# Kernel optimization log

Measured on AMD Instinct MI355X. Metric: run time of the kernel, lower is better.

Reference implementation:

```python
import jax, jax.numpy as jnp
import numpy as np

B, C, H, W = 8, 64, 64, 64
R = 4
INTER = C // R   # 16
QK = C // 8      # 8
OUT = 64
EPS = 1e-5

def _bn(h, s, b, m, v):
    # inference-mode BatchNorm2d over channel dim of NCHW
    inv = s / jnp.sqrt(v + EPS)
    return h * inv[None, :, None, None] + (b - m * inv)[None, :, None, None]

def _conv1x1(h, w, b):
    # 1x1 conv == per-pixel matmul over channels
    return jnp.einsum('oc,bchw->bohw', w, h) + b[None, :, None, None]

def setup_inputs() -> dict:
    key = jax.random.key(0)
    ks = jax.random.split(key, 16)
    def wgt(k, shape):
        return jax.random.normal(k, shape, jnp.float32) * 0.05
    ones = lambda n: jnp.ones((n,), jnp.float32)
    zeros = lambda n: jnp.zeros((n,), jnp.float32)
    return {
        'x': jax.random.normal(ks[0], (B, C, H, W), jnp.float32),
        'lw1': wgt(ks[1], (INTER, C)), 'lb1': zeros(INTER),
        'ls1': ones(INTER), 'lbb1': zeros(INTER), 'lm1': zeros(INTER), 'lv1': ones(INTER),
        'lw2': wgt(ks[2], (C, INTER)), 'lb2': zeros(C),
        'ls2': ones(C), 'lbb2': zeros(C), 'lm2': zeros(C), 'lv2': ones(C),
        'gw1': wgt(ks[3], (INTER, C)), 'gb1': zeros(INTER),
        'gs1': ones(INTER), 'gbb1': zeros(INTER), 'gm1': zeros(INTER), 'gv1': ones(INTER),
        'gw2': wgt(ks[4], (C, INTER)), 'gb2': zeros(C),
        'gs2': ones(C), 'gbb2': zeros(C), 'gm2': zeros(C), 'gv2': ones(C),
        'qw': wgt(ks[5], (QK, C)), 'qb': zeros(QK),
        'kw': wgt(ks[6], (QK, C)), 'kb': zeros(QK),
        'vw': wgt(ks[7], (C, C)), 'vb': zeros(C),
        'gamma': jnp.zeros((1,), jnp.float32),  # torch init: zeros
        'cw': wgt(ks[8], (OUT, C, 3, 3)), 'cb': zeros(OUT),
        'cs': ones(OUT), 'cbb': zeros(OUT), 'cm': zeros(OUT), 'cv': ones(OUT),
    }

def reference(x, lw1, lb1, ls1, lbb1, lm1, lv1, lw2, lb2, ls2, lbb2, lm2, lv2,
              gw1, gb1, gs1, gbb1, gm1, gv1, gw2, gb2, gs2, gbb2, gm2, gv2,
              qw, qb, kw, kb, vw, vb, gamma, cw, cb, cs, cbb, cm, cv):
    # --- SE-style channel gating: local branch (per-pixel) + global branch (GAP) ---
    xl = _bn(_conv1x1(jax.nn.relu(_bn(_conv1x1(x, lw1, lb1), ls1, lbb1, lm1, lv1)), lw2, lb2),
             ls2, lbb2, lm2, lv2)
    g = x.mean(axis=(2, 3), keepdims=True)  # AdaptiveAvgPool2d(1) -> [B,C,1,1]
    xg = _bn(_conv1x1(jax.nn.relu(_bn(_conv1x1(g, gw1, gb1), gs1, gbb1, gm1, gv1)), gw2, gb2),
             gs2, gbb2, gm2, gv2)
    xo = x * jax.nn.sigmoid(xl + xg)
    # --- full spatial self-attention (bmm -> softmax -> bmm, unscaled) ---
    # NOTE: the original forward computes this, forms gamma*out + xo, then
    # immediately overwrites `out` with conv(xo); we reproduce that faithfully.
    b_, c_, h_, w_ = x.shape
    n = h_ * w_
    q = _conv1x1(x, qw, qb).reshape(b_, QK, n)
    k = _conv1x1(x, kw, kb).reshape(b_, QK, n)
    att = jax.nn.softmax(jnp.einsum('bcn,bcm->bnm', q, k), axis=-1)  # [B,N,N]
    v = _conv1x1(x, vw, vb).reshape(b_, c_, n)
    attn_out = jnp.einsum('bcm,bnm->bcn', v, att).reshape(b_, c_, h_, w_)
    _dead = gamma[0] * attn_out + xo  # discarded by original module
    # --- final 3x3 conv + BN + ReLU applied to the gated features xo ---
    y = jax.lax.conv_general_dilated(xo, cw, (1, 1), 'SAME',
                                     dimension_numbers=('NCHW', 'OIHW', 'NCHW'))
    y = y + cb[None, :, None, None]
    return jax.nn.relu(_bn(y, cs, cbb, cm, cv))
```

## Files before the change

kernel.cpp:

```cpp
#include <hip/hip_runtime.h>
#include <hip/hip_bf16.h>

#define NPIX 4096
#define FEPS 1e-5f

typedef __hip_bfloat16 bf16;
typedef __attribute__((ext_vector_type(8))) short bf16x8;
typedef __attribute__((ext_vector_type(4))) float f32x4;

#define OFF_FOLD 64
#define OFF_G    512
#define OFF_LW1  1024
#define OFF_LW2  2048
#define OFF_GW1  3072
#define OFF_GW2  4096
#define WSWZ_BYTES_OFF 20480
#define XO_BYTES_OFF   94208

template<typename T> __device__ __forceinline__ float ldf(const T* p);
template<> __device__ __forceinline__ float ldf<bf16>(const bf16* p)  { return __bfloat162float(*p); }
template<> __device__ __forceinline__ float ldf<float>(const float* p){ return *p; }

template<typename T> __device__ __forceinline__ void stf(T* p, float v);
template<> __device__ __forceinline__ void stf<bf16>(bf16* p, float v)  { *p = __float2bfloat16(v); }
template<> __device__ __forceinline__ void stf<float>(float* p, float v){ *p = v; }

__device__ __forceinline__ unsigned short f2bu(float f) {
    union { bf16 h; unsigned short u; } c; c.h = __float2bfloat16(f); return c.u;
}
__device__ __forceinline__ float blo(unsigned u) {
    union { unsigned i; float f; } c; c.i = u << 16; return c.f;
}
__device__ __forceinline__ float bhi(unsigned u) {
    union { unsigned i; float f; } c; c.i = u & 0xffff0000u; return c.f;
}

__device__ __forceinline__ int probe_flag(const unsigned* __restrict__ x,
                                          int tid, int* sflag)
{
    if (tid < 64) {
        unsigned w = x[tid];
        unsigned h = w & 0xffffu;
        int e = (int)((h >> 7) & 0xff);
        int hit = (h == 0u || (e >= 96 && e <= 160)) ? 1 : 0;
        unsigned long long m = __ballot(hit);
        if (tid == 0) *sflag = (__popcll(m) >= 40) ? 1 : 2;
    }
    __syncthreads();
    return *sflag;
}

struct PrepArgs7 { const void* p[30]; };

template<typename T>
__device__ void prep_body(const PrepArgs7& a, float* __restrict__ ws,
                          unsigned short* __restrict__ wswz, int flag)
{
    const T* lw1  = (const T*)a.p[0];  const T* lb1  = (const T*)a.p[1];
    const T* ls1  = (const T*)a.p[2];  const T* lbb1 = (const T*)a.p[3];
    const T* lm1  = (const T*)a.p[4];  const T* lv1  = (const T*)a.p[5];
    const T* lw2  = (const T*)a.p[6];  const T* lb2  = (const T*)a.p[7];
    const T* ls2  = (const T*)a.p[8];  const T* lbb2 = (const T*)a.p[9];
    const T* lm2  = (const T*)a.p[10]; const T* lv2  = (const T*)a.p[11];
    const T* gw1  = (const T*)a.p[12]; const T* gb1  = (const T*)a.p[13];
    const T* gs1  = (const T*)a.p[14]; const T* gbb1 = (const T*)a.p[15];
    const T* gm1  = (const T*)a.p[16]; const T* gv1  = (const T*)a.p[17];
    const T* gw2  = (const T*)a.p[18]; const T* gb2  = (const T*)a.p[19];
    const T* gs2  = (const T*)a.p[20]; const T* gbb2 = (const T*)a.p[21];
    const T* gm2  = (const T*)a.p[22]; const T* gv2  = (const T*)a.p[23];
    const T* cw   = (const T*)a.p[24]; const T* cb   = (const T*)a.p[25];
    const T* cs   = (const T*)a.p[26]; const T* cbb  = (const T*)a.p[27];
    const T* cm   = (const T*)a.p[28]; const T* cv   = (const T*)a.p[29];

    int bx = blockIdx.x;
    int tid = threadIdx.x;
    if (bx < 16) {
        for (int e = tid; e < 2304; e += 256) {
            int E = bx * 2304 + e;
            int j = E & 7;
            int F = E >> 3;
            int l = F & 63;
            int g = (F >> 6) & 3;
            int ts = F >> 8;
            int s = ts & 1;
            int t = ts >> 1;
            int oc = g * 16 + (l & 15);
            int ic = s * 32 + (l >> 4) * 8 + j;
            wswz[E] = f2bu(ldf(cw + (oc * 64 + ic) * 9 + t));
        }
    } else if (bx == 16) {
        for (int e = tid; e < 4096; e += 256) {
            if (e < 1024)      ws[OFF_LW1 + e]        = ldf(lw1 + e);
            else if (e < 2048) ws[OFF_LW2 + e - 1024] = ldf(lw2 + e - 1024);
            else if (e < 3072) ws[OFF_GW1 + e - 2048] = ldf(gw1 + e - 2048);
            else               ws[OFF_GW2 + e - 3072] = ldf(gw2 + e - 3072);
        }
    } else {
        if (tid == 0) ((int*)ws)[0] = flag;
        if (tid < 16) {
            float inv = ldf(ls1 + tid) * rsqrtf(ldf(lv1 + tid) + FEPS);
            ws[OFF_FOLD + 0  + tid] = inv;
            ws[OFF_FOLD + 16 + tid] = ldf(lb1 + tid) * inv + ldf(lbb1 + tid) - ldf(lm1 + tid) * inv;
            float ginv = ldf(gs1 + tid) * rsqrtf(ldf(gv1 + tid) + FEPS);
            ws[OFF_FOLD + 160 + tid] = ginv;
            ws[OFF_FOLD + 176 + tid] = ldf(gb1 + tid) * ginv + ldf(gbb1 + tid) - ldf(gm1 + tid) * ginv;
        }
        if (tid < 64) {
            float inv2 = ldf(ls2 + tid) * rsqrtf(ldf(lv2 + tid) + FEPS);
            ws[OFF_FOLD + 32 + tid] = inv2;
            ws[OFF_FOLD + 96 + tid] = ldf(lb2 + tid) * inv2 + ldf(lbb2 + tid) - ldf(lm2 + tid) * inv2;
            float ginv2 = ldf(gs2 + tid) * rsqrtf(ldf(gv2 + tid) + FEPS);
            ws[OFF_FOLD + 192 + tid] = ginv2;
            ws[OFF_FOLD + 256 + tid] = ldf(gb2 + tid) * ginv2 + ldf(gbb2 + tid) - ldf(gm2 + tid) * ginv2;
            float cinv = ldf(cs + tid) * rsqrtf(ldf(cv + tid) + FEPS);
            ws[OFF_FOLD + 320 + tid] = cinv;
            ws[OFF_FOLD + 384 + tid] = ldf(cb + tid) * cinv + ldf(cbb + tid) - ldf(cm + tid) * cinv;
        }
    }
}

__global__ void r7_prep_means(PrepArgs7 a, const void* __restrict__ xv,
                              float* __restrict__ ws,
                              unsigned short* __restrict__ wswz)
{
    __shared__ int sflag;
    int t = threadIdx.x;
    int flag = probe_flag((const unsigned*)xv, t, &sflag);
    int bx = blockIdx.x;

    if (bx < 18) {
        if (flag == 1) prep_body<bf16>(a, ws, wswz, flag);
        else           prep_body<float>(a, ws, wswz, flag);
        return;
    }

    int bc = bx - 18;
    float s = 0.f;
    if (flag == 1) {
        const uint4* p = (const uint4*)((const bf16*)xv + (size_t)bc * NPIX);
#pragma unroll
        for (int i = 0; i < 2; ++i) {
            uint4 v = p[t * 2 + i];
            s += blo(v.x) + bhi(v.x) + blo(v.y) + bhi(v.y)
               + blo(v.z) + bhi(v.z) + blo(v.w) + bhi(v.w);
        }
    } else {
        const float4* p = (const float4*)((const float*)xv + (size_t)bc * NPIX);
#pragma unroll
        for (int i = 0; i < 4; ++i) {
            float4 v = p[t * 4 + i];
            s += v.x + v.y + v.z + v.w;
        }
    }
#pragma unroll
    for (int off = 32; off > 0; off >>= 1) s += __shfl_down(s, off, 64);
    __shared__ float red[4];
    if ((t & 63) == 0) red[t >> 6] = s;
    __syncthreads();
    if (t == 0)
        ws[OFF_G + bc] = (red[0] + red[1] + red[2] + red[3]) * (1.0f / 4096.0f);
}

__device__ void gate_slow_f32(const void* __restrict__ xv, float* __restrict__ ws,
                              uint4* __restrict__ xo)
{
    int b = blockIdx.x >> 5;
    int n = (blockIdx.x & 31) * 128 + threadIdx.x;
    int tid = threadIdx.x;

    __shared__ float t1[16];
    __shared__ float xg[64];
    if (tid < 16) {
        float s = 0.f;
#pragma unroll
        for (int c = 0; c < 64; ++c)
            s += ws[OFF_GW1 + tid * 64 + c] * ws[OFF_G + b * 64 + c];
        t1[tid] = fmaxf(ws[OFF_FOLD + 160 + tid] * s + ws[OFF_FOLD + 176 + tid], 0.f);
    }
    __syncthreads();
    if (tid < 64) {
        float s = 0.f;
#pragma unroll
        for (int j = 0; j < 16; ++j) s += ws[OFF_GW2 + tid * 16 + j] * t1[j];
        xg[tid] = ws[OFF_FOLD + 192 + tid] * s + ws[OFF_FOLD + 256 + tid];
    }
    __syncthreads();

    const float* xb = (const float*)xv + (size_t)b * 64 * NPIX + n;
    float xr[64];
#pragma unroll
    for (int c = 0; c < 64; ++c) xr[c] = xb[c * NPIX];

    float h[16];
#pragma unroll
    for (int i = 0; i < 16; ++i) {
        float s = 0.f;
#pragma unroll
        for (int c = 0; c < 64; ++c) s += ws[OFF_LW1 + i * 64 + c] * xr[c];
        h[i] = fmaxf(ws[OFF_FOLD + 0 + i] * s + ws[OFF_FOLD + 16 + i], 0.f);
    }

    uint4* xop = xo + ((size_t)b * NPIX + n) * 8;
#pragma unroll
    for (int cg = 0; cg < 8; ++cg) {
        unsigned v[8];
#pragma unroll
        for (int j = 0; j < 8; ++j) {
            int c = cg * 8 + j;
            float s = 0.f;
#pragma unroll
            for (int k = 0; k < 16; ++k) s += ws[OFF_LW2 + c * 16 + k] * h[k];
            float z = ws[OFF_FOLD + 32 + c] * s + ws[OFF_FOLD + 96 + c] + xg[c];
            v[j] = (unsigned)f2bu(xr[c] / (1.0f + __expf(-z)));
        }
        uint4 pk;
        pk.x = v[0] | (v[1] << 16);
        pk.y = v[2] | (v[3] << 16);
        pk.z = v[4] | (v[5] << 16);
        pk.w = v[6] | (v[7] << 16);
        xop[cg] = pk;
    }
}

__global__ __launch_bounds__(128)
void r7_gate(const void* __restrict__ xv, float* __restrict__ ws,
             uint4* __restrict__ xo)
{
    if (((const int*)ws)[0] != 1) { gate_slow_f32(xv, ws, xo); return; }

    int bx = blockIdx.x;
    int b = bx >> 5;
    int pix0 = (bx & 31) * 128;
    int t = threadIdx.x;

    __shared__ float t1[16];
    __shared__ float xg[64];
    __shared__ char tile[64 * 256];

    const uint4* xsrc = (const uint4*)((const bf16*)xv + (size_t)b * 64 * NPIX + pix0);
    uint4 ld[8];
#pragma unroll
    for (int k = 0; k < 8; ++k) {
        int e = k * 128 + t;
        int c = e >> 4;
        int u = e & 15;
        ld[k] = xsrc[(size_t)c * 512 + u];
    }
    if (t < 16) {
        float s = 0.f;
#pragma unroll
        for (int c = 0; c < 64; ++c)
            s += ws[OFF_GW1 + t * 64 + c] * ws[OFF_G + b * 64 + c];
        t1[t] = fmaxf(ws[OFF_FOLD + 160 + t] * s + ws[OFF_FOLD + 176 + t], 0.f);
    }
#pragma unroll
    for (int k = 0; k < 8; ++k) {
        int e = k * 128 + t;
        int c = e >> 4;
        int u = e & 15;
        *(uint4*)(tile + c * 256 + u * 16) = ld[k];
    }
    __syncthreads();
    if (t < 64) {
        float s = 0.f;
#pragma unroll
        for (int j = 0; j < 16; ++j) s += ws[OFF_GW2 + t * 16 + j] * t1[j];
        xg[t] = ws[OFF_FOLD + 192 + t] * s + ws[OFF_FOLD + 256 + t];
    }
    float xr[64];
#pragma unroll
    for (int c = 0; c < 64; ++c)
        xr[c] = __bfloat162float(*(const bf16*)(tile + c * 256 + t * 2));
    float h[16];
#pragma unroll
    for (int i = 0; i < 16; ++i) {
        float s = 0.f;
#pragma unroll
        for (int c = 0; c < 64; ++c) s += ws[OFF_LW1 + i * 64 + c] * xr[c];
        h[i] = fmaxf(ws[OFF_FOLD + 0 + i] * s + ws[OFF_FOLD + 16 + i], 0.f);
    }
    __syncthreads();
    uint4* xop = xo + ((size_t)b * NPIX + pix0 + t) * 8;
#pragma unroll
    for (int cg = 0; cg < 8; ++cg) {
        unsigned v[8];
#pragma unroll
        for (int j = 0; j < 8; ++j) {
            int c = cg * 8 + j;
            float s = 0.f;
#pragma unroll
            for (int k = 0; k < 16; ++k) s += ws[OFF_LW2 + c * 16 + k] * h[k];
            float z = ws[OFF_FOLD + 32 + c] * s + ws[OFF_FOLD + 96 + c] + xg[c];
            v[j] = (unsigned)f2bu(xr[c] / (1.0f + __expf(-z)));
        }
        uint4 pk;
        pk.x = v[0] | (v[1] << 16);
        pk.y = v[2] | (v[3] << 16);
        pk.z = v[4] | (v[5] << 16);
        pk.w = v[6] | (v[7] << 16);
        xop[cg] = pk;
    }
}

template<typename T>
__device__ void conv_body(const bf16x8* __restrict__ wsw, const float* __restrict__ ws,
                          const char* __restrict__ xob_base, void* __restrict__ outv)
{
    int bx  = blockIdx.x;
    int b   = bx >> 7;
    int r   = (bx >> 1) & 63;
    int c0  = (bx & 1) * 32;
    int tid = threadIdx.x;
    int w   = tid >> 6;
    int l   = tid & 63;
    int a   = l & 15;
    int q   = l >> 4;

    const char* xob = xob_base + (size_t)b * NPIX * 128;

    int  colOff[3][2];
    bool edge[3][2];
#pragma unroll
    for (int dci = 0; dci < 3; ++dci)
#pragma unroll
        for (int nf = 0; nf < 2; ++nf) {
            int c = c0 + nf * 16 + a + (dci - 1);
            edge[dci][nf] = (c < 0) || (c > 63);
            c = min(63, max(0, c));
            colOff[dci][nf] = c << 7;
        }

    const bf16x8 zf = {0, 0, 0, 0, 0, 0, 0, 0};
    f32x4 acc[2][2] = {};

#pragma unroll
    for (int t = 0; t < 9; ++t) {
        const int dr  = t / 3 - 1;
        const int dci = t % 3;
        int rr = r + dr;
        if (rr < 0 || rr > 63) continue;
        const char* rowp = xob + rr * 8192;
#pragma unroll
        for (int s = 0; s < 2; ++s) {
            bf16x8 A0 = wsw[((t * 2 + s) * 4 + 2 * w + 0) * 64 + l];
            bf16x8 A1 = wsw[((t * 2 + s) * 4 + 2 * w + 1) * 64 + l];
            int sq = s * 64 + q * 16;
#pragma unroll
            for (int nf = 0; nf < 2; ++nf) {
                bf16x8 B = *(const bf16x8*)(rowp + colOff[dci][nf] + sq);
                if (dci != 1) { if (edge[dci][nf]) B = zf; }
                acc[0][nf] = __builtin_amdgcn_mfma_f32_16x16x32_bf16(A0, B, acc[0][nf], 0, 0, 0);
                acc[1][nf] = __builtin_amdgcn_mfma_f32_16x16x32_bf16(A1, B, acc[1][nf], 0, 0, 0);
            }
        }
    }

    const float* cA = ws + OFF_FOLD + 320;
    const float* cB = ws + OFF_FOLD + 384;
    int pixBase = r * 64 + c0;
#pragma unroll
    for (int gi = 0; gi < 2; ++gi) {
        int g = 2 * w + gi;
#pragma unroll
        for (int reg = 0; reg < 4; ++reg) {
            int oc = g * 16 + q * 4 + reg;
            float Af = cA[oc];
            float Bf = cB[oc];
#pragma unroll
            for (int nf = 0; nf < 2; ++nf) {
                int pix = pixBase + nf * 16 + a;
                float y = fmaxf(acc[gi][nf][reg] * Af + Bf, 0.f);
                stf((T*)outv + ((size_t)b * 64 + oc) * NPIX + pix, y);
            }
        }
    }
}

__global__ __launch_bounds__(128)
void r7_conv(const bf16x8* __restrict__ wsw, const float* __restrict__ ws,
             const char* __restrict__ xob_base, void* __restrict__ outv)
{
    if (((const int*)ws)[0] == 1) conv_body<bf16>(wsw, ws, xob_base, outv);
    else                          conv_body<float>(wsw, ws, xob_base, outv);
}

extern "C" void kernel_launch(void* const* d_in, const int* in_sizes, int n_in,
                              void* d_out, int out_size, void* d_ws, size_t ws_size,
                              hipStream_t stream)
{
    (void)in_sizes; (void)n_in; (void)out_size; (void)ws_size;
    const void* x = d_in[0];
    float* ws = (float*)d_ws;
    unsigned short* wswz = (unsigned short*)((char*)d_ws + WSWZ_BYTES_OFF);
    char* xo = (char*)d_ws + XO_BYTES_OFF;

    PrepArgs7 pa;
    for (int i = 0; i < 24; ++i) pa.p[i] = d_in[1 + i];
    for (int i = 0; i < 6; ++i)  pa.p[24 + i] = d_in[32 + i];

    r7_prep_means<<<dim3(530), dim3(256), 0, stream>>>(pa, x, ws, wswz);
    r7_gate<<<dim3(256), dim3(128), 0, stream>>>(x, ws, (uint4*)xo);
    r7_conv<<<dim3(1024), dim3(128), 0, stream>>>(
        (const bf16x8*)wswz, ws, xo, d_out);
}
```

Baseline: 182.4 us.

## Stage conv input halo in swizzled LDS and coalesce gate output stores

The 3x3 conv kernel now cooperatively loads the three input rows plus a one-pixel column halo into XOR-swizzled shared memory, with zero padding written in, and reads its MFMA B operands from there instead of issuing repeated global loads with edge masks. The gate kernel packs its bf16 outputs through a swizzled LDS tile so the global writes are contiguous across threads rather than strided per pixel. This targets redundant and uncoalesced global traffic, at the cost of extra barriers and shared-memory footprint. The probe-flag edit is a no-op rewrite.

```diff
diff --git a/kernel.cpp b/kernel.cpp
--- a/kernel.cpp
+++ b/kernel.cpp
@@ -42,7 +42,8 @@
         unsigned w = x[tid];
         unsigned h = w & 0xffffu;
         int e = (int)((h >> 7) & 0xff);
-        int hit = (h == 0u || (e >= 96 && e <= 160)) ? 1 : 0;
+        int hit = (h == 0u || (e >= 96 && e <= 160)) ? 1 : 2;
+        hit = (hit == 1) ? 1 : 0;
         unsigned long long m = __ballot(hit);
         if (tid == 0) *sflag = (__popcll(m) >= 40) ? 1 : 2;
     }
@@ -280,7 +281,6 @@
         h[i] = fmaxf(ws[OFF_FOLD + 0 + i] * s + ws[OFF_FOLD + 16 + i], 0.f);
     }
     __syncthreads();
-    uint4* xop = xo + ((size_t)b * NPIX + pix0 + t) * 8;
 #pragma unroll
     for (int cg = 0; cg < 8; ++cg) {
         unsigned v[8];
@@ -298,13 +298,25 @@
         pk.y = v[2] | (v[3] << 16);
         pk.z = v[4] | (v[5] << 16);
         pk.w = v[6] | (v[7] << 16);
-        xop[cg] = pk;
-    }
-}
+        *(uint4*)(tile + ((t * 128 + cg * 16) ^ ((t & 7) << 4))) = pk;
+    }
+    __syncthreads();
+    uint4* xop = xo + ((size_t)b * NPIX + pix0) * 8;
+#pragma unroll
+    for (int k = 0; k < 8; ++k) {
+        int e = k * 128 + t;
+        int p = e >> 3;
+        int u = e & 7;
+        xop[e] = *(const uint4*)(tile + ((p * 128 + u * 16) ^ ((p & 7) << 4)));
+    }
+}
+
+#define CONV_LDS_BYTES (3 * 34 * 128)
 
 template<typename T>
 __device__ void conv_body(const bf16x8* __restrict__ wsw, const float* __restrict__ ws,
-                          const char* __restrict__ xob_base, void* __restrict__ outv)
+                          const char* __restrict__ xob_base, void* __restrict__ outv,
+                          char* __restrict__ lds)
 {
     int bx  = blockIdx.x;
     int b   = bx >> 7;
@@ -318,19 +330,23 @@
 
     const char* xob = xob_base + (size_t)b * NPIX * 128;
 
-    int  colOff[3][2];
-    bool edge[3][2];
-#pragma unroll
-    for (int dci = 0; dci < 3; ++dci)
-#pragma unroll
-        for (int nf = 0; nf < 2; ++nf) {
-            int c = c0 + nf * 16 + a + (dci - 1);
-            edge[dci][nf] = (c < 0) || (c > 63);
-            c = min(63, max(0, c));
-            colOff[dci][nf] = c << 7;
-        }
-
-    const bf16x8 zf = {0, 0, 0, 0, 0, 0, 0, 0};
+    for (int e = tid; e < 816; e += 128) {
+        int row = e / 272;
+        int rm  = e - row * 272;
+        int px  = rm >> 3;
+        int u   = rm & 7;
+        int col = c0 - 1 + px;
+        int rr  = r - 1 + row;
+        uint4 v = {0u, 0u, 0u, 0u};
+        if (col >= 0 && col <= 63) {
+            int rc = min(63, max(0, rr));
+            v = *(const uint4*)(xob + rc * 8192 + col * 128 + u * 16);
+        }
+        int byt = ((row * 34 + px) * 128 + u * 16) ^ ((px & 7) << 4);
+        *(uint4*)(lds + byt) = v;
+    }
+    __syncthreads();
+
     f32x4 acc[2][2] = {};
 
 #pragma unroll
@@ -339,7 +355,7 @@
         const int dci = t % 3;
         int rr = r + dr;
         if (rr < 0 || rr > 63) continue;
-        const char* rowp = xob + rr * 8192;
+        const char* rowp = lds + (dr + 1) * (34 * 128);
 #pragma unroll
         for (int s = 0; s < 2; ++s) {
             bf16x8 A0 = wsw[((t * 2 + s) * 4 + 2 * w + 0) * 64 + l];
@@ -347,8 +363,9 @@
             int sq = s * 64 + q * 16;
 #pragma unroll
             for (int nf = 0; nf < 2; ++nf) {
-                bf16x8 B = *(const bf16x8*)(rowp + colOff[dci][nf] + sq);
-                if (dci != 1) { if (edge[dci][nf]) B = zf; }
+                int tp  = nf * 16 + a + dci;
+                int byt = tp * 128 + (sq ^ ((tp & 7) << 4));
+                bf16x8 B = *(const bf16x8*)(rowp + byt);
                 acc[0][nf] = __builtin_amdgcn_mfma_f32_16x16x32_bf16(A0, B, acc[0][nf], 0, 0, 0);
                 acc[1][nf] = __builtin_amdgcn_mfma_f32_16x16x32_bf16(A1, B, acc[1][nf], 0, 0, 0);
             }
@@ -380,8 +397,9 @@
 void r7_conv(const bf16x8* __restrict__ wsw, const float* __restrict__ ws,
              const char* __restrict__ xob_base, void* __restrict__ outv)
 {
-    if (((const int*)ws)[0] == 1) conv_body<bf16>(wsw, ws, xob_base, outv);
-    else                          conv_body<float>(wsw, ws, xob_base, outv);
+    __shared__ char lds[CONV_LDS_BYTES];
+    if (((const int*)ws)[0] == 1) conv_body<bf16>(wsw, ws, xob_base, outv, lds);
+    else                          conv_body<float>(wsw, ws, xob_base, outv, lds);
 }
 
 extern "C" void kernel_launch(void* const* d_in, const int* in_sizes, int n_in,
```

After: 177.6 us. 2.6% less time.
